# Optimization experiments

Measured on AMD Instinct MI355X. Metric: run time of the kernel, lower is better.

Reference implementation:

```python
import jax, jax.numpy as jnp
import numpy as np

N_NODES = 10000
N_EDGES = 160000
F_IN = 2613
D = 256
H = 4
NEG_SLOPE = 0.2
BN_EPS = 1e-5


def _bn(h, g, b):
    # BatchNorm1d in training mode: batch statistics, biased variance
    return (h - h.mean(0)) / jnp.sqrt(h.var(0) + BN_EPS) * g + b


def _gat_conv(h_in, src, dst, n, W, att_src, att_dst, bias):
    # PyG GATConv, concat=True: h_in [n, F] -> [n, H*D]
    h = (h_in @ W).reshape(n, H, D)                      # [n, H, D]
    a_src = jnp.sum(h * att_src, axis=-1)                # [n, H]
    a_dst = jnp.sum(h * att_dst, axis=-1)                # [n, H]
    e = jax.nn.leaky_relu(a_src[src] + a_dst[dst], NEG_SLOPE)  # [E, H]
    # segment softmax over destination nodes (stable)
    m = jax.ops.segment_max(e, dst, num_segments=n)
    e = jnp.exp(e - m[dst])
    denom = jax.ops.segment_sum(e, dst, num_segments=n)
    alpha = e / (denom[dst] + 1e-16)                     # [E, H]
    out = jax.ops.segment_sum(h[src] * alpha[:, :, None], dst, num_segments=n)
    return out.reshape(n, H * D) + bias


def setup_inputs() -> dict:
    key = jax.random.key(0)
    ks = jax.random.split(key, 24)
    s = 0.02
    inp = {
        "x": jax.random.normal(ks[0], (N_NODES, F_IN), jnp.float32),
        "edges": jax.random.randint(ks[1], (2, N_EDGES), 0, N_NODES, jnp.int64),
        # MLP stack
        "W1": jax.random.normal(ks[2], (F_IN, D), jnp.float32) * s,
        "b1": jnp.zeros((D,), jnp.float32),
        "W2": jax.random.normal(ks[3], (D, D), jnp.float32) * s,
        "b2": jnp.zeros((D,), jnp.float32),
        "W3": jax.random.normal(ks[4], (D, D), jnp.float32) * s,
        "b3": jnp.zeros((D,), jnp.float32),
        # BatchNorm affine params
        "g1": jnp.ones((D,), jnp.float32), "be1": jnp.zeros((D,), jnp.float32),
        "g2": jnp.ones((D,), jnp.float32), "be2": jnp.zeros((D,), jnp.float32),
        "g3": jnp.ones((D,), jnp.float32), "be3": jnp.zeros((D,), jnp.float32),
        "g4": jnp.ones((H * D,), jnp.float32), "be4": jnp.zeros((H * D,), jnp.float32),
        "Wg1": jax.random.normal(ks[5], (D, H * D), jnp.float32) * s,
        "as1": jax.random.normal(ks[6], (H, D), jnp.float32) * s,
        "ad1": jax.random.normal(ks[7], (H, D), jnp.float32) * s,
        "bg1": jnp.zeros((H * D,), jnp.float32),
        "Wg2": jax.random.normal(ks[8], (H * D, H * D), jnp.float32) * s,
        "as2": jax.random.normal(ks[9], (H, D), jnp.float32) * s,
        "ad2": jax.random.normal(ks[10], (H, D), jnp.float32) * s,
        "bg2": jnp.zeros((H * D,), jnp.float32),
    }
    return inp


def reference(x, edges, W1, b1, W2, b2, W3, b3,
              g1, be1, g2, be2, g3, be3, g4, be4,
              Wg1, as1, ad1, bg1, Wg2, as2, ad2, bg2):
    n = x.shape[0]
    src, dst = edges[0], edges[1]
    # PyG: remove existing self-loops then add one per node. We reroute
    # accidental self-loops deterministically, then append self-loops.
    dst = jnp.where(src == dst, (dst + 1) % n, dst)
    loops = jnp.arange(n, dtype=src.dtype)
    src = jnp.concatenate([src, loops])
    dst = jnp.concatenate([dst, loops])

    h = jax.nn.elu(_bn(x @ W1 + b1, g1, be1))
    h = jax.nn.elu(_bn(h @ W2 + b2, g2, be2))
    h = jax.nn.elu(_bn(h @ W3 + b3, g3, be3))
    h = _gat_conv(h, src, dst, n, Wg1, as1, ad1, bg1)
    h = jax.nn.elu(_bn(h, g4, be4))
    h = _gat_conv(h, src, dst, n, Wg2, as2, ad2, bg2)
    return h
```

## Files before the change

kernel.cpp:

```cpp
#include <hip/hip_runtime.h>
#include <hip/hip_bf16.h>

typedef __attribute__((ext_vector_type(8))) short short8v;
typedef __attribute__((ext_vector_type(4))) float f32x4;

__device__ inline float b2f(ushort u) {
  union { uint i; float f; } c;
  c.i = (uint)u << 16;
  return c.f;
}
__device__ inline ushort f2b(float f) {
  __hip_bfloat16 h = __float2bfloat16(f);
  return *(ushort*)&h;
}

typedef __attribute__((address_space(1))) const unsigned int guint;
typedef __attribute__((address_space(3))) unsigned int luint;
__device__ __forceinline__ void gload16(const void* g, void* l) {
  __builtin_amdgcn_global_load_lds((guint*)g, (luint*)l, 16, 0, 0);
}

template <bool BN, bool ALIGNED>
__global__ __launch_bounds__(256) void gemm_bn(
    const float* __restrict__ A, const __hip_bfloat16* __restrict__ Bh,
    const __hip_bfloat16* __restrict__ Bl, const float* __restrict__ sc,
    const float* __restrict__ sh, float* __restrict__ P, int M, int N, int K,
    int Kp, int nc, int nr, int nz) {
  __shared__ ushort Ash[128][40];
  __shared__ ushort Asl[128][40];
  __shared__ ushort Bs2[128][32];
  __shared__ ushort Bl2[128][32];
  const int nwg = gridDim.x;
  const int b = blockIdx.x;
  const int l = (b & 7) * (nwg >> 3) + (b >> 3);
  const int cb = l % nc;
  const int rr = (l / nc) % nr;
  const int z = l / (nc * nr);

  const int tid = threadIdx.x;
  const int lane = tid & 63;
  const int w = tid >> 6, wr = w >> 1, wc = w & 1;
  const int brow = rr * 128, bcol = cb * 128;
  const int l15 = lane & 15, koff = (lane >> 4) * 8;
  const int arow = tid >> 1, aseg = (tid & 1) * 16;
  const int srow = tid >> 2, sseg = (tid & 3) * 8;
  const int nK = (K + 31) >> 5;
  const int ks0 = (nK * z) / nz, ks1 = (nK * (z + 1)) / nz;

  f32x4 acc[4][4] = {};

  const int ar = brow + arow;
  const bool arv = ar < M;
  const float* Arow = A + (long)ar * K;
  const ushort* gBh0 = (const ushort*)Bh + (long)(bcol + srow) * Kp + sseg;
  const ushort* gBh1 = (const ushort*)Bh + (long)(bcol + 64 + srow) * Kp + sseg;
  const ushort* gBl0 = (const ushort*)Bl + (long)(bcol + srow) * Kp + sseg;
  const ushort* gBl1 = (const ushort*)Bl + (long)(bcol + 64 + srow) * Kp + sseg;
  ushort* lBh0 = &Bs2[0][0] + ((w * 64) << 3);
  ushort* lBh1 = &Bs2[0][0] + ((256 + w * 64) << 3);
  ushort* lBl0 = &Bl2[0][0] + ((w * 64) << 3);
  ushort* lBl1 = &Bl2[0][0] + ((256 + w * 64) << 3);

  for (int ks = ks0; ks < ks1; ++ks) {
    const int k0 = ks << 5;
    const int kbase = k0 + aseg;
    float av[16];
    if (arv) {
      if (ALIGNED) {
        const float4* ap = (const float4*)(Arow + kbase);
#pragma unroll
        for (int q = 0; q < 4; ++q) {
          float4 f = ap[q];
          av[q * 4 + 0] = f.x;
          av[q * 4 + 1] = f.y;
          av[q * 4 + 2] = f.z;
          av[q * 4 + 3] = f.w;
        }
      } else {
        if (kbase + 16 <= K) {
#pragma unroll
          for (int j = 0; j < 16; ++j) av[j] = Arow[kbase + j];
        } else {
#pragma unroll
          for (int j = 0; j < 16; ++j)
            av[j] = (kbase + j < K) ? Arow[kbase + j] : 0.f;
        }
      }
      if (BN) {
#pragma unroll
        for (int q = 0; q < 4; ++q) {
          float4 c4 = *(const float4*)(sc + kbase + q * 4);
          float4 h4 = *(const float4*)(sh + kbase + q * 4);
          float* a4 = &av[q * 4];
          a4[0] = fmaf(a4[0], c4.x, h4.x);
          a4[1] = fmaf(a4[1], c4.y, h4.y);
          a4[2] = fmaf(a4[2], c4.z, h4.z);
          a4[3] = fmaf(a4[3], c4.w, h4.w);
        }
#pragma unroll
        for (int j = 0; j < 16; ++j) {
          float v = av[j];
          av[j] = v > 0.f ? v : (__expf(v) - 1.f);
        }
      }
    } else {
#pragma unroll
      for (int j = 0; j < 16; ++j) av[j] = 0.f;
    }
    short8v ah0, ah1, al0, al1;
#pragma unroll
    for (int j = 0; j < 8; ++j) {
      {
        uint u = __float_as_uint(av[j]);
        ah0[j] = (short)(u >> 16);
        al0[j] = (short)f2b(av[j] - __uint_as_float(u & 0xFFFF0000u));
      }
      {
        uint u = __float_as_uint(av[j + 8]);
        ah1[j] = (short)(u >> 16);
        al1[j] = (short)f2b(av[j + 8] - __uint_as_float(u & 0xFFFF0000u));
      }
    }
    __syncthreads();
    gload16(gBh0 + k0, lBh0);
    gload16(gBh1 + k0, lBh1);
    gload16(gBl0 + k0, lBl0);
    gload16(gBl1 + k0, lBl1);
    *(short8v*)&Ash[arow][aseg] = ah0;
    *(short8v*)&Ash[arow][aseg + 8] = ah1;
    *(short8v*)&Asl[arow][aseg] = al0;
    *(short8v*)&Asl[arow][aseg + 8] = al1;
    __syncthreads();

    short8v bfh[4], bfl[4];
#pragma unroll
    for (int nn = 0; nn < 4; ++nn) {
      bfh[nn] = *(const short8v*)&Bs2[wc * 64 + nn * 16 + l15][koff];
      bfl[nn] = *(const short8v*)&Bl2[wc * 64 + nn * 16 + l15][koff];
    }
#pragma unroll
    for (int m = 0; m < 4; ++m) {
      short8v afh = *(const short8v*)&Ash[wr * 64 + m * 16 + l15][koff];
      short8v afl = *(const short8v*)&Asl[wr * 64 + m * 16 + l15][koff];
#pragma unroll
      for (int nn = 0; nn < 4; ++nn) {
        acc[m][nn] = __builtin_amdgcn_mfma_f32_16x16x32_bf16(afh, bfh[nn], acc[m][nn], 0, 0, 0);
        acc[m][nn] = __builtin_amdgcn_mfma_f32_16x16x32_bf16(afh, bfl[nn], acc[m][nn], 0, 0, 0);
        acc[m][nn] = __builtin_amdgcn_mfma_f32_16x16x32_bf16(afl, bfh[nn], acc[m][nn], 0, 0, 0);
      }
    }
  }

  float* outp = P + (long)z * M * N;
#pragma unroll
  for (int m = 0; m < 4; ++m) {
#pragma unroll
    for (int nn = 0; nn < 4; ++nn) {
      int col = bcol + wc * 64 + nn * 16 + l15;
#pragma unroll
      for (int r = 0; r < 4; ++r) {
        int row = brow + wr * 64 + m * 16 + (lane >> 4) * 4 + r;
        if (row < M) outp[(long)row * N + col] = acc[m][nn][r];
      }
    }
  }
}

__global__ __launch_bounds__(256) void gemm_bf16(
    const ushort* __restrict__ A, const __hip_bfloat16* __restrict__ B,
    ushort* __restrict__ C, int M, int N, int K, int nc, int nr) {
  __shared__ ushort A2[128][32];
  __shared__ ushort B2[128][32];
  const int nwg = gridDim.x;
  const int b = blockIdx.x;
  const int l = (b & 7) * (nwg >> 3) + (b >> 3);
  const int cb = l % nc;
  const int rr = l / nc;

  const int tid = threadIdx.x;
  const int lane = tid & 63;
  const int w = tid >> 6, wr = w >> 1, wc = w & 1;
  const int brow = rr * 128, bcol = cb * 128;
  const int l15 = lane & 15, koff = (lane >> 4) * 8;
  const int srow = tid >> 2, sseg = (tid & 3) * 8;
  const int nK = K >> 5;

  f32x4 acc[4][4] = {};

  const ushort* gA0 = A + (long)(brow + srow) * K + sseg;
  const ushort* gA1 = A + (long)(brow + 64 + srow) * K + sseg;
  const ushort* gB0 = (const ushort*)B + (long)(bcol + srow) * K + sseg;
  const ushort* gB1 = (const ushort*)B + (long)(bcol + 64 + srow) * K + sseg;
  ushort* lA0 = &A2[0][0] + ((w * 64) << 3);
  ushort* lA1 = &A2[0][0] + ((256 + w * 64) << 3);
  ushort* lB0 = &B2[0][0] + ((w * 64) << 3);
  ushort* lB1 = &B2[0][0] + ((256 + w * 64) << 3);

  for (int ks = 0; ks < nK; ++ks) {
    const int k0 = ks << 5;
    __syncthreads();
    gload16(gA0 + k0, lA0);
    gload16(gA1 + k0, lA1);
    gload16(gB0 + k0, lB0);
    gload16(gB1 + k0, lB1);
    __syncthreads();

    short8v bf[4];
#pragma unroll
    for (int nn = 0; nn < 4; ++nn)
      bf[nn] = *(const short8v*)&B2[wc * 64 + nn * 16 + l15][koff];
#pragma unroll
    for (int m = 0; m < 4; ++m) {
      short8v af = *(const short8v*)&A2[wr * 64 + m * 16 + l15][koff];
#pragma unroll
      for (int nn = 0; nn < 4; ++nn)
        acc[m][nn] = __builtin_amdgcn_mfma_f32_16x16x32_bf16(af, bf[nn], acc[m][nn], 0, 0, 0);
    }
  }

#pragma unroll
  for (int m = 0; m < 4; ++m) {
#pragma unroll
    for (int nn = 0; nn < 4; ++nn) {
      int col = bcol + wc * 64 + nn * 16 + l15;
#pragma unroll
      for (int r = 0; r < 4; ++r) {
        int row = brow + wr * 64 + m * 16 + (lane >> 4) * 4 + r;
        if (row < M) C[(long)row * N + col] = f2b(acc[m][nn][r]);
      }
    }
  }
}

__global__ __launch_bounds__(256) void bn_elu_b16(
    const float* __restrict__ h, const float* __restrict__ sc,
    const float* __restrict__ sh, ushort* __restrict__ o, long MN, int N) {
  long nq = MN >> 2;
  for (long q = blockIdx.x * 256LL + threadIdx.x; q < nq;
       q += (long)gridDim.x * 256LL) {
    long i = q << 2;
    int col = (int)(i % N);
    float4 v = *(const float4*)(h + i);
    float4 c = *(const float4*)(sc + col);
    float4 s = *(const float4*)(sh + col);
    float a0 = fmaf(v.x, c.x, s.x);
    float a1 = fmaf(v.y, c.y, s.y);
    float a2 = fmaf(v.z, c.z, s.z);
    float a3 = fmaf(v.w, c.w, s.w);
    a0 = a0 > 0.f ? a0 : (__expf(a0) - 1.f);
    a1 = a1 > 0.f ? a1 : (__expf(a1) - 1.f);
    a2 = a2 > 0.f ? a2 : (__expf(a2) - 1.f);
    a3 = a3 > 0.f ? a3 : (__expf(a3) - 1.f);
    ushort4 r;
    r.x = f2b(a0);
    r.y = f2b(a1);
    r.z = f2b(a2);
    r.w = f2b(a3);
    *(ushort4*)(o + i) = r;
  }
}

template <bool BIAS, bool STATS>
__global__ __launch_bounds__(256) void reduce_post(
    const float* __restrict__ P, const float* __restrict__ bias,
    float* __restrict__ C, float* __restrict__ osum, float* __restrict__ osq,
    long MN, int N, int Z) {
  const int col = (int)((blockIdx.x * 256 + threadIdx.x) % N);
  const float bv = BIAS ? bias[col] : 0.f;
  float ps = 0.f, pq = 0.f;
  for (long i = blockIdx.x * 256LL + threadIdx.x; i < MN;
       i += (long)gridDim.x * 256LL) {
    float s = bv;
    for (int zz = 0; zz < Z; ++zz) s += P[(long)zz * MN + i];
    C[i] = s;
    if (STATS) {
      ps += s;
      pq += s * s;
    }
  }
  if (STATS) {
    atomicAdd(&osum[col], ps);
    atomicAdd(&osq[col], pq);
  }
}

__global__ __launch_bounds__(256) void bn_coef(
    const float* __restrict__ ssum, const float* __restrict__ ssq,
    const float* __restrict__ g, const float* __restrict__ be,
    float* __restrict__ sc, float* __restrict__ sh, int N, float invM) {
  int c = blockIdx.x * 256 + threadIdx.x;
  if (c >= N) return;
  float mean = ssum[c] * invM;
  float var = ssq[c] * invM - mean * mean;
  float s = rsqrtf(var + 1e-5f) * g[c];
  sc[c] = s;
  sh[c] = be[c] - mean * s;
}

template <bool LO>
__global__ __launch_bounds__(256) void trans_split(
    const float* __restrict__ W, __hip_bfloat16* __restrict__ Oh,
    __hip_bfloat16* __restrict__ Ol, int K, int N, int Kp) {
  __shared__ float tile[64][65];
  const int k0 = blockIdx.x * 64, n0 = blockIdx.y * 64;
  const int tx = threadIdx.x & 63, ty = threadIdx.x >> 6;
#pragma unroll
  for (int j = 0; j < 16; ++j) {
    int r = ty * 16 + j;
    int k = k0 + r;
    tile[r][tx] = (k < K) ? W[(long)k * N + n0 + tx] : 0.f;
  }
  __syncthreads();
#pragma unroll
  for (int j = 0; j < 16; ++j) {
    int a = ty * 16 + j;
    float v = tile[tx][a];
    long o = (long)(n0 + a) * Kp + k0 + tx;
    if (LO) {
      uint u = __float_as_uint(v);
      ushort hu = (ushort)(u >> 16);
      Oh[o] = *(__hip_bfloat16*)&hu;
      ushort lu = f2b(v - __uint_as_float(u & 0xFFFF0000u));
      Ol[o] = *(__hip_bfloat16*)&lu;
    } else {
      ushort hu = f2b(v);
      Oh[o] = *(__hip_bfloat16*)&hu;
    }
  }
}

__global__ __launch_bounds__(256) void bn_stats(
    const float* __restrict__ h, int M, int N, float* __restrict__ sum,
    float* __restrict__ sumsq) {
  int col = blockIdx.y * 256 + threadIdx.x;
  float s = 0.f, sq = 0.f;
  for (int r = blockIdx.x; r < M; r += gridDim.x) {
    float v = h[(long)r * N + col];
    s += v;
    sq += v * v;
  }
  atomicAdd(&sum[col], s);
  atomicAdd(&sumsq[col], sq);
}

__global__ __launch_bounds__(256) void att_scores_bf16(
    const ushort* __restrict__ hgb, const float* __restrict__ att_s,
    const float* __restrict__ att_d, float* __restrict__ a_src,
    float* __restrict__ a_dst, int n) {
  int node = blockIdx.x;
  int h = threadIdx.x >> 6, lane = threadIdx.x & 63;
  int c = lane * 4;
  ushort4 hv = *(const ushort4*)(hgb + (long)node * 1024 + h * 256 + c);
  float4 as = *(const float4*)(att_s + h * 256 + c);
  float4 ad = *(const float4*)(att_d + h * 256 + c);
  float x0 = b2f(hv.x), x1 = b2f(hv.y), x2 = b2f(hv.z), x3 = b2f(hv.w);
  float ss = x0 * as.x + x1 * as.y + x2 * as.z + x3 * as.w;
  float sd = x0 * ad.x + x1 * ad.y + x2 * ad.z + x3 * ad.w;
#pragma unroll
  for (int off = 32; off; off >>= 1) {
    ss += __shfl_down(ss, off);
    sd += __shfl_down(sd, off);
  }
  if (lane == 0) {
    a_src[node * 4 + h] = ss;
    a_dst[node * 4 + h] = sd;
  }
}

__global__ __launch_bounds__(256) void deg_count(
    const int* __restrict__ srcA, const int* __restrict__ dstA,
    int* __restrict__ deg, int n, int E0, int E) {
  int e = blockIdx.x * blockDim.x + threadIdx.x;
  if (e >= E) return;
  int d;
  if (e < E0) {
    int s = srcA[e];
    d = dstA[e];
    if (s == d) d = (d + 1) % n;
  } else {
    d = e - E0;
  }
  atomicAdd(&deg[d], 1);
}

__global__ __launch_bounds__(256) void scan_rows(
    const int* __restrict__ deg, int* __restrict__ row_start, int n) {
  __shared__ int sums[256];
  int t = threadIdx.x;
  int chunk = (n + 255) / 256;
  int start = t * chunk, end = min(start + chunk, n);
  int s = 0;
  for (int i = start; i < end; ++i) s += deg[i];
  sums[t] = s;
  __syncthreads();
  for (int off = 1; off < 256; off <<= 1) {
    int v = (t >= off) ? sums[t - off] : 0;
    __syncthreads();
    sums[t] += v;
    __syncthreads();
  }
  int run = (t == 0) ? 0 : sums[t - 1];
  for (int i = start; i < end; ++i) {
    row_start[i] = run;
    run += deg[i];
  }
  if (t == 255) row_start[n] = run;
}

__global__ __launch_bounds__(256) void scatter_edges(
    const int* __restrict__ srcA, const int* __restrict__ dstA,
    int* __restrict__ cursor, int* __restrict__ csr_src, int n, int E0, int E) {
  int e = blockIdx.x * blockDim.x + threadIdx.x;
  if (e >= E) return;
  int s, d;
  if (e < E0) {
    s = srcA[e];
    d = dstA[e];
    if (s == d) d = (d + 1) % n;
  } else {
    s = d = e - E0;
  }
  int pos = atomicAdd(&cursor[d], 1);
  csr_src[pos] = s;
}

__global__ __launch_bounds__(256) void aggregate_fused(
    const ushort* __restrict__ hgb, const int* __restrict__ row_start,
    const int* __restrict__ csr_src, const float* __restrict__ a_src,
    const float* __restrict__ a_dst, const float* __restrict__ bias,
    float* __restrict__ out) {
  int d = blockIdx.x;
  int t = threadIdx.x;
  int hh = t >> 6;
  int off = hh * 256 + (t & 63) * 4;
  int p0 = row_start[d], p1 = row_start[d + 1];
  float adv = a_dst[d * 4 + hh];
  float den = 1e-16f;
  float4 acc = {0.f, 0.f, 0.f, 0.f};
  for (int p = p0; p < p1; ++p) {
    int s = csr_src[p];
    float v = a_src[s * 4 + hh] + adv;
    v = v > 0.f ? v : 0.2f * v;
    float ex = __expf(v);
    den += ex;
    ushort4 hv = *(const ushort4*)(hgb + (long)s * 1024 + off);
    acc.x += ex * b2f(hv.x);
    acc.y += ex * b2f(hv.y);
    acc.z += ex * b2f(hv.z);
    acc.w += ex * b2f(hv.w);
  }
  float rden = 1.f / den;
  float4 bv = *(const float4*)(bias + off);
  float4 o;
  o.x = bv.x + acc.x * rden;
  o.y = bv.y + acc.y * rden;
  o.z = bv.z + acc.z * rden;
  o.w = bv.w + acc.w * rden;
  *(float4*)(out + (long)d * 1024 + off) = o;
}

extern "C" void kernel_launch(void* const* d_in, const int* in_sizes, int n_in,
                              void* d_out, int out_size, void* d_ws,
                              size_t ws_size, hipStream_t stream) {
  const float* x = (const float*)d_in[0];
  const int* edges = (const int*)d_in[1];
  const float* W1 = (const float*)d_in[2];
  const float* b1 = (const float*)d_in[3];
  const float* W2 = (const float*)d_in[4];
  const float* b2 = (const float*)d_in[5];
  const float* W3 = (const float*)d_in[6];
  const float* b3 = (const float*)d_in[7];
  const float* g1 = (const float*)d_in[8];
  const float* be1 = (const float*)d_in[9];
  const float* g2 = (const float*)d_in[10];
  const float* be2 = (const float*)d_in[11];
  const float* g3 = (const float*)d_in[12];
  const float* be3 = (const float*)d_in[13];
  const float* g4 = (const float*)d_in[14];
  const float* be4 = (const float*)d_in[15];
  const float* Wg1 = (const float*)d_in[16];
  const float* as1 = (const float*)d_in[17];
  const float* ad1 = (const float*)d_in[18];
  const float* bg1 = (const float*)d_in[19];
  const float* Wg2 = (const float*)d_in[20];
  const float* as2 = (const float*)d_in[21];
  const float* ad2 = (const float*)d_in[22];
  const float* bg2 = (const float*)d_in[23];
  float* out = (float*)d_out;

  const int n = 10000, E0 = 160000, E = 170000;
  const int F = 2613, Fp = 2624, D = 256, HD = 1024;
  const int* srcA = edges;
  const int* dstA = edges + E0;

  uint8_t* p = (uint8_t*)d_ws;
  auto alloc = [&](size_t bytes) -> void* {
    void* r = (void*)p;
    p += (bytes + 255) & ~(size_t)255;
    return r;
  };
  float* h1 = (float*)alloc((size_t)n * D * 4);
  float* h2 = (float*)alloc((size_t)n * D * 4);
  float* h3 = (float*)alloc((size_t)n * D * 4);
  float* agg = (float*)alloc((size_t)n * HD * 4);
  float* pbuf = (float*)alloc((size_t)8 * n * D * 4);
  ushort* hgb = (ushort*)alloc((size_t)n * HD * 2);
  ushort* actb = (ushort*)alloc((size_t)n * HD * 2);
  __hip_bfloat16* W1h = (__hip_bfloat16*)alloc((size_t)D * Fp * 2);
  __hip_bfloat16* W1l = (__hip_bfloat16*)alloc((size_t)D * Fp * 2);
  __hip_bfloat16* W2h = (__hip_bfloat16*)alloc((size_t)D * D * 2);
  __hip_bfloat16* W2l = (__hip_bfloat16*)alloc((size_t)D * D * 2);
  __hip_bfloat16* W3h = (__hip_bfloat16*)alloc((size_t)D * D * 2);
  __hip_bfloat16* W3l = (__hip_bfloat16*)alloc((size_t)D * D * 2);
  __hip_bfloat16* Wg1h = (__hip_bfloat16*)alloc((size_t)HD * D * 2);
  __hip_bfloat16* Wg2h = (__hip_bfloat16*)alloc((size_t)HD * HD * 2);
  float* asrc = (float*)alloc((size_t)n * 4 * 4);
  float* adst = (float*)alloc((size_t)n * 4 * 4);
  float* sc1 = (float*)alloc(D * 4);
  float* sh1 = (float*)alloc(D * 4);
  float* sc2 = (float*)alloc(D * 4);
  float* sh2 = (float*)alloc(D * 4);
  float* sc3 = (float*)alloc(D * 4);
  float* sh3 = (float*)alloc(D * 4);
  float* sc4 = (float*)alloc(HD * 4);
  float* sh4 = (float*)alloc(HD * 4);
  int* row_start = (int*)alloc((size_t)(n + 1) * 4);
  int* cursor = (int*)alloc((size_t)n * 4);
  int* csr_src = (int*)alloc((size_t)E * 4);
  uint8_t* z0 = p;
  float* ssum1 = (float*)alloc(D * 4);
  float* ssq1 = (float*)alloc(D * 4);
  float* ssum2 = (float*)alloc(D * 4);
  float* ssq2 = (float*)alloc(D * 4);
  float* ssum3 = (float*)alloc(D * 4);
  float* ssq3 = (float*)alloc(D * 4);
  float* ssum4 = (float*)alloc(HD * 4);
  float* ssq4 = (float*)alloc(HD * 4);
  int* deg = (int*)alloc((size_t)n * 4);
  size_t zbytes = (size_t)(p - z0);

  dim3 blk(256);
  const int rb = (n + 127) / 128;
  const int eb = (E + 255) / 256;
  const long MN_D = (long)n * D;
  const long MN_HD = (long)n * HD;
  const float invM = 1.f / (float)n;
  const int gL1 = 2 * rb * 8;
  const int gMLP = 2 * rb * 4;
  const int gGAT = 8 * rb;

  hipMemsetAsync(z0, 0, zbytes, stream);

  deg_count<<<eb, blk, 0, stream>>>(srcA, dstA, deg, n, E0, E);
  scan_rows<<<1, blk, 0, stream>>>(deg, row_start, n);
  hipMemcpyAsync(cursor, row_start, n * sizeof(int), hipMemcpyDeviceToDevice, stream);
  scatter_edges<<<eb, blk, 0, stream>>>(srcA, dstA, cursor, csr_src, n, E0, E);

  trans_split<true><<<dim3(Fp / 64, D / 64), blk, 0, stream>>>(W1, W1h, W1l, F, D, Fp);
  trans_split<true><<<dim3(D / 64, D / 64), blk, 0, stream>>>(W2, W2h, W2l, D, D, D);
  trans_split<true><<<dim3(D / 64, D / 64), blk, 0, stream>>>(W3, W3h, W3l, D, D, D);
  trans_split<false><<<dim3(D / 64, HD / 64), blk, 0, stream>>>(Wg1, Wg1h, nullptr, D, HD, D);
  trans_split<false><<<dim3(HD / 64, HD / 64), blk, 0, stream>>>(Wg2, Wg2h, nullptr, HD, HD, HD);

  gemm_bn<false, false><<<gL1, blk, 0, stream>>>(
      x, W1h, W1l, nullptr, nullptr, pbuf, n, D, F, Fp, 2, rb, 8);
  reduce_post<true, true><<<512, blk, 0, stream>>>(pbuf, b1, h1, ssum1, ssq1, MN_D, D, 8);
  bn_coef<<<1, blk, 0, stream>>>(ssum1, ssq1, g1, be1, sc1, sh1, D, invM);

  gemm_bn<true, true><<<gMLP, blk, 0, stream>>>(
      h1, W2h, W2l, sc1, sh1, pbuf, n, D, D, D, 2, rb, 4);
  reduce_post<true, true><<<512, blk, 0, stream>>>(pbuf, b2, h2, ssum2, ssq2, MN_D, D, 4);
  bn_coef<<<1, blk, 0, stream>>>(ssum2, ssq2, g2, be2, sc2, sh2, D, invM);

  gemm_bn<true, true><<<gMLP, blk, 0, stream>>>(
      h2, W3h, W3l, sc2, sh2, pbuf, n, D, D, D, 2, rb, 4);
  reduce_post<true, true><<<512, blk, 0, stream>>>(pbuf, b3, h3, ssum3, ssq3, MN_D, D, 4);
  bn_coef<<<1, blk, 0, stream>>>(ssum3, ssq3, g3, be3, sc3, sh3, D, invM);

  bn_elu_b16<<<1024, blk, 0, stream>>>(h3, sc3, sh3, actb, MN_D, D);
  gemm_bf16<<<gGAT, blk, 0, stream>>>(actb, Wg1h, hgb, n, HD, D, 8, rb);
  att_scores_bf16<<<n, blk, 0, stream>>>(hgb, as1, ad1, asrc, adst, n);
  aggregate_fused<<<n, blk, 0, stream>>>(hgb, row_start, csr_src, asrc, adst, bg1, agg);

  bn_stats<<<dim3(64, HD / 256), blk, 0, stream>>>(agg, n, HD, ssum4, ssq4);
  bn_coef<<<4, blk, 0, stream>>>(ssum4, ssq4, g4, be4, sc4, sh4, HD, invM);
  bn_elu_b16<<<2048, blk, 0, stream>>>(agg, sc4, sh4, actb, MN_HD, HD);

  gemm_bf16<<<gGAT, blk, 0, stream>>>(actb, Wg2h, hgb, n, HD, HD, 8, rb);
  att_scores_bf16<<<n, blk, 0, stream>>>(hgb, as2, ad2, asrc, adst, n);
  aggregate_fused<<<n, blk, 0, stream>>>(hgb, row_start, csr_src, asrc, adst, bg2, out);
}
```

Baseline: 572.8 us.

## Double-buffer LDS tiles and prefetch next K-slice in both GEMM kernels

Both GEMM kernels now keep two LDS buffers for their B tiles, and gemm_bf16 does the same for its A tiles. The next K-slice is fetched with global_load_lds while the current slice is being multiplied. In gemm_bn the fp32 A values for the next slice are also loaded into registers ahead of time, and the BN/ELU transform is applied only at use. The goal is to hide global-load latency behind the MFMA work and to remove one barrier per iteration in gemm_bf16. In exchange, LDS usage roughly doubles, register pressure goes up, and overlap may be limited if the compiler's waitcnt placement serializes the loads anyway.

Result: faster. 560.9 us (-2.1%).

```diff
diff --git a/kernel.cpp b/kernel.cpp
--- a/kernel.cpp
+++ b/kernel.cpp
@@ -28,8 +28,8 @@
     int Kp, int nc, int nr, int nz) {
   __shared__ ushort Ash[128][40];
   __shared__ ushort Asl[128][40];
-  __shared__ ushort Bs2[128][32];
-  __shared__ ushort Bl2[128][32];
+  __shared__ ushort Bs2[2][128][32];
+  __shared__ ushort Bl2[2][128][32];
   const int nwg = gridDim.x;
   const int b = blockIdx.x;
   const int l = (b & 7) * (nwg >> 3) + (b >> 3);
@@ -56,18 +56,15 @@
   const ushort* gBh1 = (const ushort*)Bh + (long)(bcol + 64 + srow) * Kp + sseg;
   const ushort* gBl0 = (const ushort*)Bl + (long)(bcol + srow) * Kp + sseg;
   const ushort* gBl1 = (const ushort*)Bl + (long)(bcol + 64 + srow) * Kp + sseg;
-  ushort* lBh0 = &Bs2[0][0] + ((w * 64) << 3);
-  ushort* lBh1 = &Bs2[0][0] + ((256 + w * 64) << 3);
-  ushort* lBl0 = &Bl2[0][0] + ((w * 64) << 3);
-  ushort* lBl1 = &Bl2[0][0] + ((256 + w * 64) << 3);
-
-  for (int ks = ks0; ks < ks1; ++ks) {
-    const int k0 = ks << 5;
-    const int kbase = k0 + aseg;
-    float av[16];
+  const int lo0 = (w * 64) << 3;
+  const int lo1 = (256 + w * 64) << 3;
+
+  float av[16];
+  auto loadAv = [&](int ks) {
+    const int kb = (ks << 5) + aseg;
     if (arv) {
       if (ALIGNED) {
-        const float4* ap = (const float4*)(Arow + kbase);
+        const float4* ap = (const float4*)(Arow + kb);
 #pragma unroll
         for (int q = 0; q < 4; ++q) {
           float4 f = ap[q];
@@ -77,35 +74,48 @@
           av[q * 4 + 3] = f.w;
         }
       } else {
-        if (kbase + 16 <= K) {
-#pragma unroll
-          for (int j = 0; j < 16; ++j) av[j] = Arow[kbase + j];
+        if (kb + 16 <= K) {
+#pragma unroll
+          for (int j = 0; j < 16; ++j) av[j] = Arow[kb + j];
         } else {
 #pragma unroll
-          for (int j = 0; j < 16; ++j)
-            av[j] = (kbase + j < K) ? Arow[kbase + j] : 0.f;
+          for (int j = 0; j < 16; ++j) av[j] = (kb + j < K) ? Arow[kb + j] : 0.f;
         }
       }
-      if (BN) {
-#pragma unroll
-        for (int q = 0; q < 4; ++q) {
-          float4 c4 = *(const float4*)(sc + kbase + q * 4);
-          float4 h4 = *(const float4*)(sh + kbase + q * 4);
-          float* a4 = &av[q * 4];
-          a4[0] = fmaf(a4[0], c4.x, h4.x);
-          a4[1] = fmaf(a4[1], c4.y, h4.y);
-          a4[2] = fmaf(a4[2], c4.z, h4.z);
-          a4[3] = fmaf(a4[3], c4.w, h4.w);
-        }
-#pragma unroll
-        for (int j = 0; j < 16; ++j) {
-          float v = av[j];
-          av[j] = v > 0.f ? v : (__expf(v) - 1.f);
-        }
-      }
     } else {
 #pragma unroll
       for (int j = 0; j < 16; ++j) av[j] = 0.f;
+    }
+  };
+
+  if (ks0 < ks1) {
+    loadAv(ks0);
+    const int k0 = ks0 << 5;
+    gload16(gBh0 + k0, &Bs2[0][0][0] + lo0);
+    gload16(gBh1 + k0, &Bs2[0][0][0] + lo1);
+    gload16(gBl0 + k0, &Bl2[0][0][0] + lo0);
+    gload16(gBl1 + k0, &Bl2[0][0][0] + lo1);
+  }
+
+  for (int ks = ks0; ks < ks1; ++ks) {
+    const int cur = (ks - ks0) & 1;
+    const int kbase = (ks << 5) + aseg;
+    if (BN && arv) {
+#pragma unroll
+      for (int q = 0; q < 4; ++q) {
+        float4 c4 = *(const float4*)(sc + kbase + q * 4);
+        float4 h4 = *(const float4*)(sh + kbase + q * 4);
+        float* a4 = &av[q * 4];
+        a4[0] = fmaf(a4[0], c4.x, h4.x);
+        a4[1] = fmaf(a4[1], c4.y, h4.y);
+        a4[2] = fmaf(a4[2], c4.z, h4.z);
+        a4[3] = fmaf(a4[3], c4.w, h4.w);
+      }
+#pragma unroll
+      for (int j = 0; j < 16; ++j) {
+        float v = av[j];
+        av[j] = v > 0.f ? v : (__expf(v) - 1.f);
+      }
     }
     short8v ah0, ah1, al0, al1;
 #pragma unroll
@@ -122,21 +132,27 @@
       }
     }
     __syncthreads();
-    gload16(gBh0 + k0, lBh0);
-    gload16(gBh1 + k0, lBh1);
-    gload16(gBl0 + k0, lBl0);
-    gload16(gBl1 + k0, lBl1);
     *(short8v*)&Ash[arow][aseg] = ah0;
     *(short8v*)&Ash[arow][aseg + 8] = ah1;
     *(short8v*)&Asl[arow][aseg] = al0;
     *(short8v*)&Asl[arow][aseg + 8] = al1;
     __syncthreads();
-
+    if (ks + 1 < ks1) {
+      const int k0n = (ks + 1) << 5;
+      const int nxt = cur ^ 1;
+      ushort* bh = &Bs2[nxt][0][0];
+      ushort* bl = &Bl2[nxt][0][0];
+      gload16(gBh0 + k0n, bh + lo0);
+      gload16(gBh1 + k0n, bh + lo1);
+      gload16(gBl0 + k0n, bl + lo0);
+      gload16(gBl1 + k0n, bl + lo1);
+      loadAv(ks + 1);
+    }
     short8v bfh[4], bfl[4];
 #pragma unroll
     for (int nn = 0; nn < 4; ++nn) {
-      bfh[nn] = *(const short8v*)&Bs2[wc * 64 + nn * 16 + l15][koff];
-      bfl[nn] = *(const short8v*)&Bl2[wc * 64 + nn * 16 + l15][koff];
+      bfh[nn] = *(const short8v*)&Bs2[cur][wc * 64 + nn * 16 + l15][koff];
+      bfl[nn] = *(const short8v*)&Bl2[cur][wc * 64 + nn * 16 + l15][koff];
     }
 #pragma unroll
     for (int m = 0; m < 4; ++m) {
@@ -169,8 +185,8 @@
 __global__ __launch_bounds__(256) void gemm_bf16(
     const ushort* __restrict__ A, const __hip_bfloat16* __restrict__ B,
     ushort* __restrict__ C, int M, int N, int K, int nc, int nr) {
-  __shared__ ushort A2[128][32];
-  __shared__ ushort B2[128][32];
+  __shared__ ushort A2[2][128][32];
+  __shared__ ushort B2[2][128][32];
   const int nwg = gridDim.x;
   const int b = blockIdx.x;
   const int l = (b & 7) * (nwg >> 3) + (b >> 3);
@@ -191,27 +207,32 @@
   const ushort* gA1 = A + (long)(brow + 64 + srow) * K + sseg;
   const ushort* gB0 = (const ushort*)B + (long)(bcol + srow) * K + sseg;
   const ushort* gB1 = (const ushort*)B + (long)(bcol + 64 + srow) * K + sseg;
-  ushort* lA0 = &A2[0][0] + ((w * 64) << 3);
-  ushort* lA1 = &A2[0][0] + ((256 + w * 64) << 3);
-  ushort* lB0 = &B2[0][0] + ((w * 64) << 3);
-  ushort* lB1 = &B2[0][0] + ((256 + w * 64) << 3);
+  const int lo0 = (w * 64) << 3;
+  const int lo1 = (256 + w * 64) << 3;
+
+  gload16(gA0, &A2[0][0][0] + lo0);
+  gload16(gA1, &A2[0][0][0] + lo1);
+  gload16(gB0, &B2[0][0][0] + lo0);
+  gload16(gB1, &B2[0][0][0] + lo1);
 
   for (int ks = 0; ks < nK; ++ks) {
-    const int k0 = ks << 5;
+    const int cur = ks & 1;
     __syncthreads();
-    gload16(gA0 + k0, lA0);
-    gload16(gA1 + k0, lA1);
-    gload16(gB0 + k0, lB0);
-    gload16(gB1 + k0, lB1);
-    __syncthreads();
-
+    if (ks + 1 < nK) {
+      const int k0n = (ks + 1) << 5;
+      const int nxt = cur ^ 1;
+      gload16(gA0 + k0n, &A2[nxt][0][0] + lo0);
+      gload16(gA1 + k0n, &A2[nxt][0][0] + lo1);
+      gload16(gB0 + k0n, &B2[nxt][0][0] + lo0);
+      gload16(gB1 + k0n, &B2[nxt][0][0] + lo1);
+    }
     short8v bf[4];
 #pragma unroll
     for (int nn = 0; nn < 4; ++nn)
-      bf[nn] = *(const short8v*)&B2[wc * 64 + nn * 16 + l15][koff];
+      bf[nn] = *(const short8v*)&B2[cur][wc * 64 + nn * 16 + l15][koff];
 #pragma unroll
     for (int m = 0; m < 4; ++m) {
-      short8v af = *(const short8v*)&A2[wr * 64 + m * 16 + l15][koff];
+      short8v af = *(const short8v*)&A2[cur][wr * 64 + m * 16 + l15][koff];
 #pragma unroll
       for (int nn = 0; nn < 4; ++nn)
         acc[m][nn] = __builtin_amdgcn_mfma_f32_16x16x32_bf16(af, bf[nn], acc[m][nn], 0, 0, 0);
```
